# Kernel optimization log

Hardware: AMD Instinct MI355X
Metric: run time of the kernel (lower is better)

Reference implementation:

```python
import jax, jax.numpy as jnp
import numpy as np

B, T, J, D_O = 32, 128, 16, 16
D, H, L, M = 256, 8, 4, 8
DH = D // H
GMAX = 5
MLP = 4 * D
NUM_JOINT = np.array([16, 12, 10, 14, 16, 8, 12, 16])
NUM_GLOBAL = np.array([4, 0, 3, 5, 2, 0, 4, 3])


def setup_inputs() -> dict:
    key = jax.random.key(0)
    it = iter(jax.random.split(key, 48))
    def nrm(shape, s):
        return jax.random.normal(next(it), shape, dtype=jnp.float32) * s
    obs = jax.random.normal(next(it), (B, T, J, D_O), dtype=jnp.float32)
    jtype = jax.random.randint(next(it), (B, T, J), 0, 3)
    slide_mask = jtype == 0
    hinge_mask = jtype == 1
    global_mask = jtype == 2
    act_mask = jax.random.randint(next(it), (B, T, J), 0, 2).astype(bool)
    morph_mask = jax.random.randint(next(it), (B, J, J), 0, 2).astype(bool) | jnp.eye(J, dtype=bool)[None]
    m_idx = jax.random.randint(next(it), (B,), 0, M)
    has_global = jnp.asarray(NUM_GLOBAL > 0)
    s = 0.02
    W_slide = nrm((2, D), s); b_slide = jnp.zeros((D,), jnp.float32)
    W_hinge = nrm((3, D), s); b_hinge = jnp.zeros((D,), jnp.float32)
    # per-morphology global projection, rows beyond num_global zeroed (padding)
    grow = jnp.arange(GMAX)[None, :] < jnp.asarray(NUM_GLOBAL)[:, None]
    W_global = nrm((M, GMAX, D), s) * grow[:, :, None]
    b_global = jnp.zeros((M, D), jnp.float32)
    W_act = nrm((1, D), s)  # actuator_embedding: Linear(1, D, bias=False)
    # per-morphology position embeddings, zero beyond num_joint (matches torch zeros init + slice assign)
    jrow = jnp.arange(J)[None, :] < jnp.asarray(NUM_JOINT)[:, None]
    pos_emb = nrm((M, J, D), 1.0) * jrow[:, :, None]
    ln1_w = jnp.ones((L, D), jnp.float32); ln1_b = jnp.zeros((L, D), jnp.float32)
    qkv_w = nrm((L, D, 3 * D), s); qkv_b = jnp.zeros((L, 3 * D), jnp.float32)
    proj_w = nrm((L, D, D), s); proj_b = jnp.zeros((L, D), jnp.float32)
    ln2_w = jnp.ones((L, D), jnp.float32); ln2_b = jnp.zeros((L, D), jnp.float32)
    fc1_w = nrm((L, D, MLP), s); fc1_b = jnp.zeros((L, MLP), jnp.float32)
    fc2_w = nrm((L, MLP, D), s); fc2_b = jnp.zeros((L, D), jnp.float32)
    ls1 = jnp.full((L, D), 1e-4, jnp.float32); ls2 = jnp.full((L, D), 1e-4, jnp.float32)
    return dict(obs=obs, slide_mask=slide_mask, hinge_mask=hinge_mask, global_mask=global_mask,
                act_mask=act_mask, morph_mask=morph_mask, m_idx=m_idx, has_global=has_global,
                W_slide=W_slide, b_slide=b_slide, W_hinge=W_hinge, b_hinge=b_hinge,
                W_global=W_global, b_global=b_global, W_act=W_act, pos_emb=pos_emb,
                ln1_w=ln1_w, ln1_b=ln1_b, qkv_w=qkv_w, qkv_b=qkv_b, proj_w=proj_w, proj_b=proj_b,
                ln2_w=ln2_w, ln2_b=ln2_b, fc1_w=fc1_w, fc1_b=fc1_b, fc2_w=fc2_w, fc2_b=fc2_b,
                ls1=ls1, ls2=ls2)


def _ln(x, w, b):
    m = x.mean(-1, keepdims=True)
    v = ((x - m) ** 2).mean(-1, keepdims=True)
    return (x - m) * jax.lax.rsqrt(v + 1e-5) * w + b


def reference(obs, slide_mask, hinge_mask, global_mask, act_mask, morph_mask, m_idx, has_global,
              W_slide, b_slide, W_hinge, b_hinge, W_global, b_global, W_act, pos_emb,
              ln1_w, ln1_b, qkv_w, qkv_b, proj_w, proj_b, ln2_w, ln2_b,
              fc1_w, fc1_b, fc2_w, fc2_b, ls1, ls2):
    # --- JointEmbedding (morphology-indexed expert selection, vectorized gather) ---
    emb_slide = obs[..., :2] @ W_slide + b_slide
    x = jnp.where(slide_mask[..., None], emb_slide, jnp.zeros_like(emb_slide))
    emb_hinge = obs[..., :3] @ W_hinge + b_hinge
    x = jnp.where(hinge_mask[..., None], emb_hinge, x)
    # per-sample expert weights gathered by m_idx; padded cols are zero so math matches per-expert in-dims
    emb_g = jnp.einsum('btjg,bgd->btjd', obs[..., :GMAX], W_global[m_idx]) + b_global[m_idx][:, None, None, :]
    gmask = global_mask & has_global[m_idx][:, None, None]  # experts with num_global==0 are skipped
    x = jnp.where(gmask[..., None], emb_g, x)
    # actuator embedding: Linear(1, D, bias=False) on 0/1 mask
    x = x + act_mask[..., None].astype(x.dtype) * W_act[0]
    # morphology-indexed position embedding (zero-padded beyond num_joint)
    x = x + pos_emb[m_idx][:, None]  # (B,1,J,D) broadcast over T
    # --- masked transformer over joints; (B T) flattening == broadcasting mask over T ---
    bias = jnp.where(morph_mask, 0.0, -1e9).astype(x.dtype)[:, None, None, :, :]  # (B,1,1,J,J)
    for l in range(L):
        h = _ln(x, ln1_w[l], ln1_b[l])
        qkv = h @ qkv_w[l] + qkv_b[l]
        q, k, v = jnp.split(qkv, 3, axis=-1)
        def heads(t):
            return t.reshape(B, T, J, H, DH).transpose(0, 1, 3, 2, 4)
        q, k, v = heads(q), heads(k), heads(v)
        scores = jnp.einsum('bthqd,bthkd->bthqk', q, k) * (DH ** -0.5) + bias
        a = jax.nn.softmax(scores, axis=-1)
        o = jnp.einsum('bthqk,bthkd->bthqd', a, v).transpose(0, 1, 3, 2, 4).reshape(B, T, J, D)
        x = x + ls1[l] * (o @ proj_w[l] + proj_b[l])
        h = _ln(x, ln2_w[l], ln2_b[l])
        x = x + ls2[l] * (jax.nn.gelu(h @ fc1_w[l] + fc1_b[l]) @ fc2_w[l] + fc2_b[l])
    return x
```

## Files before the change

### kernel.cpp

```cpp
#include <hip/hip_runtime.h>
#include <hip/hip_bf16.h>
#include <stdint.h>

typedef short bf16x8 __attribute__((ext_vector_type(8)));
typedef float f32x4 __attribute__((ext_vector_type(4)));

#define DI __device__ __forceinline__

DI unsigned short f2bf(float f) {
    return __builtin_bit_cast(unsigned short, __float2bfloat16(f));
}

DI f32x4 mfma16(bf16x8 a, bf16x8 b, f32x4 c) {
    return __builtin_amdgcn_mfma_f32_16x16x32_bf16(a, b, c, 0, 0, 0);
}

DI void gload16(const unsigned short* g, unsigned short* l) {
    __builtin_amdgcn_global_load_lds(
        (const __attribute__((address_space(1))) unsigned int*)g,
        (__attribute__((address_space(3))) unsigned int*)l, 16, 0, 0);
}

DI float gelu_f(float hv) {
    float y = 0.7978845608028654f * (hv + 0.044715f * hv * hv * hv);
    float th = 1.0f - 2.0f / (__expf(2.0f * y) + 1.0f);
    return 0.5f * hv * (1.0f + th);
}

#define RSYNC4() do { asm volatile("s_waitcnt vmcnt(4)" ::: "memory"); \
    __builtin_amdgcn_s_barrier(); __builtin_amdgcn_sched_barrier(0); } while (0)
#define RSYNC0() do { asm volatile("s_waitcnt vmcnt(0)" ::: "memory"); \
    __builtin_amdgcn_s_barrier(); __builtin_amdgcn_sched_barrier(0); } while (0)

__global__ __launch_bounds__(256)
void prep_kernel(const float* __restrict__ qkv_w, const float* __restrict__ proj_w,
                 const float* __restrict__ fc1_w, const float* __restrict__ fc2_w,
                 const float* __restrict__ ls1, const float* __restrict__ ls2,
                 unsigned short* __restrict__ out)
{
    __shared__ float tileA[256][17];
    __shared__ float tileB[32][129];
    const int tid = threadIdx.x;
    const int tgl = blockIdx.x;
    const int layer = tgl / 192;
    const int tl = tgl % 192;
    bool kindA; const float* W; int ldN = 0, src_n16 = 0, strip = 0, ctb = 0;
    const float* lsp = nullptr;
    if (tl < 64) {
        int h = tl >> 3, u = tl & 7;
        if (u < 6) { kindA = true;  W = qkv_w + (size_t)layer * 256 * 768; ldN = 768;
                     src_n16 = (u >> 1) * 16 + 2 * h + (u & 1); }
        else       { kindA = false; W = proj_w + (size_t)layer * 256 * 256; ldN = 256;
                     strip = 32 * h; ctb = (u - 6) * 8; lsp = ls1 + layer * 256; }
    } else {
        int q = tl - 64, rp = q >> 2, v = q & 3;
        if (v < 2) { kindA = true;  W = fc1_w + (size_t)layer * 256 * 1024; ldN = 1024;
                     src_n16 = 2 * rp + v; }
        else       { kindA = false; W = fc2_w + (size_t)layer * 1024 * 256; ldN = 256;
                     strip = 32 * rp; ctb = (v - 2) * 8; lsp = ls2 + layer * 256; }
    }
    if (kindA) {
        const int cn = tid & 15, k0 = tid >> 4;
        const float* src = W + src_n16 * 16 + cn;
        #pragma unroll
        for (int p = 0; p < 16; ++p) {
            int kk = p * 16 + k0;
            tileA[kk][cn] = src[(size_t)kk * ldN];
        }
    } else {
        const int kk = tid >> 3, c0 = (tid & 7) * 16;
        const float* src = W + (size_t)(strip + kk) * ldN + ctb * 16 + c0;
        #pragma unroll
        for (int j = 0; j < 16; ++j) tileB[kk][c0 + j] = src[j];
    }
    __syncthreads();
    unsigned short* dst = out + (size_t)tgl * 4096;
    {
        int e0 = tid * 16;
        int s = e0 >> 9;
        int l = (e0 >> 3) & 63;
        union { unsigned short u[8]; bf16x8 v; } pk;
        if (kindA) {
            int kb = 32 * s + 8 * (l >> 4);
            int n = l & 15;
            #pragma unroll
            for (int i = 0; i < 8; ++i) pk.u[i] = f2bf(tileA[kb + i][n]);
        } else {
            int kb = 8 * (l >> 4);
            int cc = s * 16 + (l & 15);
            const float sc = lsp[ctb * 16 + cc];
            #pragma unroll
            for (int i = 0; i < 8; ++i) pk.u[i] = f2bf(tileB[kb + i][cc] * sc);
        }
        *(bf16x8*)(dst + e0) = pk.v;
        int e1 = e0 + 8;
        int s1 = e1 >> 9;
        int l1 = (e1 >> 3) & 63;
        union { unsigned short u[8]; bf16x8 v; } pk1;
        if (kindA) {
            int kb = 32 * s1 + 8 * (l1 >> 4);
            int n = l1 & 15;
            #pragma unroll
            for (int i = 0; i < 8; ++i) pk1.u[i] = f2bf(tileA[kb + i][n]);
        } else {
            int kb = 8 * (l1 >> 4);
            int cc = s1 * 16 + (l1 & 15);
            const float sc = lsp[ctb * 16 + cc];
            #pragma unroll
            for (int i = 0; i < 8; ++i) pk1.u[i] = f2bf(tileB[kb + i][cc] * sc);
        }
        *(bf16x8*)(dst + e1) = pk1.v;
    }
}

#define CAT_(a, b) a##b
#define CAT(a, b) CAT_(a, b)

#define F8N(F)      F(0)F(1)F(2)F(3)F(4)F(5)F(6)F(7)
#define F16N(F)     F(0)F(1)F(2)F(3)F(4)F(5)F(6)F(7)F(8)F(9)F(10)F(11)F(12)F(13)F(14)F(15)
#define F8A(F,a)    F(0,a)F(1,a)F(2,a)F(3,a)F(4,a)F(5,a)F(6,a)F(7,a)
#define F8H(F,a)    F(8,a)F(9,a)F(10,a)F(11,a)F(12,a)F(13,a)F(14,a)F(15,a)
#define F16A(F,a)   F8A(F,a) F8H(F,a)
#define F8B(F,a,b)  F(0,a,b)F(1,a,b)F(2,a,b)F(3,a,b)F(4,a,b)F(5,a,b)F(6,a,b)F(7,a,b)
#define F16C(F,a,b) F8B(F,a,b) F(8,a,b)F(9,a,b)F(10,a,b)F(11,a,b)F(12,a,b)F(13,a,b)F(14,a,b)F(15,a,b)
#define F16D(F,a,b,c) F(0,a,b,c)F(1,a,b,c)F(2,a,b,c)F(3,a,b,c)F(4,a,b,c)F(5,a,b,c)F(6,a,b,c)F(7,a,b,c)F(8,a,b,c)F(9,a,b,c)F(10,a,b,c)F(11,a,b,c)F(12,a,b,c)F(13,a,b,c)F(14,a,b,c)F(15,a,b,c)

#define DECLX(n)  f32x4 CAT(xA,n);
#define DECLAV(s) bf16x8 CAT(avA,s);

#define EMB_N(n, P, R) { const int col = (n)*16 + lq; float e = 0.f;            \
    if (sl_) e = o0_*W_slide[col] + o1_*W_slide[256+col] + b_slide[col];        \
    else if (hi_) e = o0_*W_hinge[col] + o1_*W_hinge[256+col]                   \
                    + o2_*W_hinge[512+col] + b_hinge[col];                      \
    else if (gl_) e = b_global[m*256+col]                                       \
        + o0_*W_global[(m*5+0)*256+col] + o1_*W_global[(m*5+1)*256+col]         \
        + o2_*W_global[(m*5+2)*256+col] + o3_*W_global[(m*5+3)*256+col]         \
        + o4_*W_global[(m*5+4)*256+col];                                        \
    if (am_) e += W_act[col];                                                   \
    e += pos_emb[pb_ + col];                                                    \
    CAT(CAT(x,P),n)[R] = e; }

#define EMB_ROW(R, G, P) { const int j_ = lg*4 + (R);                           \
    const size_t tok_ = (size_t)(G)*16 + j_;                                    \
    const float* ob_ = obs + tok_*16;                                           \
    const float o0_=ob_[0], o1_=ob_[1], o2_=ob_[2], o3_=ob_[3], o4_=ob_[4];     \
    const int sl_=slide_m[tok_], hi_=hinge_m[tok_];                             \
    const int gl_=global_m[tok_]&&hg; const int am_=act_m[tok_];                \
    const size_t pb_ = ((size_t)m*16+j_)*256;                                   \
    F16C(EMB_N, P, R) }

#define EMBED(G, P) { EMB_ROW(0,G,P) EMB_ROW(1,G,P) EMB_ROW(2,G,P) EMB_ROW(3,G,P) }

#define LNS_N(n, P) { f32x4 v4_ = CAT(CAT(x,P),n);                              \
    sm0+=v4_[0]; sq0+=v4_[0]*v4_[0]; sm1+=v4_[1]; sq1+=v4_[1]*v4_[1];           \
    sm2+=v4_[2]; sq2+=v4_[2]*v4_[2]; sm3+=v4_[3]; sq3+=v4_[3]*v4_[3]; }

#define RED4(v) { v+=__shfl_xor(v,1,64); v+=__shfl_xor(v,2,64);                 \
                  v+=__shfl_xor(v,4,64); v+=__shfl_xor(v,8,64); }

#define LNW_N(n, P) { const float wv_=lw_[(n)*16+lq], lbv_=lb_[(n)*16+lq];      \
    const int t16_=(2*(n)+(lq>>3))&3; const int base_=(((n)&7)>>1)*512+(lq&7);  \
    slotA[base_+(4*lg+0+16*t16_)*8] = f2bf((CAT(CAT(x,P),n)[0]-mu0)*rs0*wv_+lbv_); \
    slotA[base_+(4*lg+1+16*t16_)*8] = f2bf((CAT(CAT(x,P),n)[1]-mu1)*rs1*wv_+lbv_); \
    slotA[base_+(4*lg+2+16*t16_)*8] = f2bf((CAT(CAT(x,P),n)[2]-mu2)*rs2*wv_+lbv_); \
    slotA[base_+(4*lg+3+16*t16_)*8] = f2bf((CAT(CAT(x,P),n)[3]-mu3)*rs3*wv_+lbv_); }

#define LAYER_NORM(LW, LB, P) do {                                              \
    const float* lw_ = (LW); const float* lb_ = (LB);                           \
    float sm0=0,sm1=0,sm2=0,sm3=0, sq0=0,sq1=0,sq2=0,sq3=0;                     \
    F16A(LNS_N, P)                                                              \
    RED4(sm0) RED4(sm1) RED4(sm2) RED4(sm3)                                     \
    RED4(sq0) RED4(sq1) RED4(sq2) RED4(sq3)                                     \
    const float mu0=sm0*(1.f/256.f), mu1=sm1*(1.f/256.f);                       \
    const float mu2=sm2*(1.f/256.f), mu3=sm3*(1.f/256.f);                       \
    const float rs0=rsqrtf(sq0*(1.f/256.f)-mu0*mu0+1e-5f);                      \
    const float rs1=rsqrtf(sq1*(1.f/256.f)-mu1*mu1+1e-5f);                      \
    const float rs2=rsqrtf(sq2*(1.f/256.f)-mu2*mu2+1e-5f);                      \
    const float rs3=rsqrtf(sq3*(1.f/256.f)-mu3*mu3+1e-5f);                      \
    F8A(LNW_N, P)                                                               \
    CAT(CAT(av,P),0) = *(const bf16x8*)(slotA + 0*512 + lane*8);                \
    CAT(CAT(av,P),1) = *(const bf16x8*)(slotA + 1*512 + lane*8);                \
    CAT(CAT(av,P),2) = *(const bf16x8*)(slotA + 2*512 + lane*8);                \
    CAT(CAT(av,P),3) = *(const bf16x8*)(slotA + 3*512 + lane*8);                \
    F8H(LNW_N, P)                                                               \
    CAT(CAT(av,P),4) = *(const bf16x8*)(slotA + 0*512 + lane*8);                \
    CAT(CAT(av,P),5) = *(const bf16x8*)(slotA + 1*512 + lane*8);                \
    CAT(CAT(av,P),6) = *(const bf16x8*)(slotA + 2*512 + lane*8);                \
    CAT(CAT(av,P),7) = *(const bf16x8*)(slotA + 3*512 + lane*8);                \
} while (0)

#define MFKE(s, BUFK, TT) { ae = mfma16(CAT(avA,s), bfrag((BUFK),(TT),(s)), ae); }
#define MFKO(s, BUFK, TT) { aod = mfma16(CAT(avA,s), bfrag((BUFK),(TT),(s)), aod); }
#define MFK8(BUFK, TT) MFKE(0,BUFK,TT) MFKO(1,BUFK,TT) MFKE(2,BUFK,TT) MFKO(3,BUFK,TT) \
                       MFKE(4,BUFK,TT) MFKO(5,BUFK,TT) MFKE(6,BUFK,TT) MFKO(7,BUFK,TT)

#define FOLD_CT(ct, BUFK, OFS, OF) {                                            \
    bf16x8 bq_ = bfrag((BUFK), 2 + ((ct)>>3), (ct)&7);                          \
    CAT(xA,ct) = mfma16((OF), bq_, CAT(xA,ct)); }

#define ADDB_N(n, OFS, BP) { const float d_ = ls_lds[(OFS)+(n)*16+lq]*(BP)[(n)*16+lq]; \
    CAT(xA,n)[0]+=d_; CAT(xA,n)[1]+=d_; CAT(xA,n)[2]+=d_; CAT(xA,n)[3]+=d_; }

#define STORE_N(n) {                                                            \
    op0[(lg*4+0)*256+(n)*16+lq]=CAT(xA,n)[0]; op0[(lg*4+1)*256+(n)*16+lq]=CAT(xA,n)[1]; \
    op0[(lg*4+2)*256+(n)*16+lq]=CAT(xA,n)[2]; op0[(lg*4+3)*256+(n)*16+lq]=CAT(xA,n)[3]; }

__global__ __launch_bounds__(512)
void fused_kernel(const float* __restrict__ obs, const int* __restrict__ slide_m,
                  const int* __restrict__ hinge_m, const int* __restrict__ global_m,
                  const int* __restrict__ act_m, const int* __restrict__ morph_m,
                  const int* __restrict__ m_idx, const int* __restrict__ has_g,
                  const float* __restrict__ W_slide, const float* __restrict__ b_slide,
                  const float* __restrict__ W_hinge, const float* __restrict__ b_hinge,
                  const float* __restrict__ W_global, const float* __restrict__ b_global,
                  const float* __restrict__ W_act, const float* __restrict__ pos_emb,
                  const float* __restrict__ ln1_w, const float* __restrict__ ln1_b,
                  const float* __restrict__ qkv_b, const float* __restrict__ proj_b,
                  const float* __restrict__ ln2_w, const float* __restrict__ ln2_b,
                  const float* __restrict__ fc1_b, const float* __restrict__ fc2_b,
                  const float* __restrict__ ls1, const float* __restrict__ ls2,
                  const unsigned short* __restrict__ wsb, float* __restrict__ out)
{
    __shared__ __align__(16) unsigned char smem[157696];
    unsigned short* dbuf = (unsigned short*)smem;
    float* ls4 = (float*)(smem + 98304);
    float* bias_lds = (float*)(smem + 106496);
    float* biasbuf = (float*)(smem + 107520);
    const int tid = threadIdx.x;
    const int w = tid >> 6, lane = tid & 63, lq = lane & 15, lg = lane >> 4;
    unsigned char* pw = smem + 114688 + w * 5376;
    unsigned short* slotA = (unsigned short*)pw;
    unsigned short* qp = (unsigned short*)pw;
    unsigned short* ks = (unsigned short*)(pw + 1280);
    unsigned short* vT = (unsigned short*)(pw + 2560);

    const int G = blockIdx.x * 8 + w;
    const int b = blockIdx.x >> 4;
    const int m = m_idx[b];
    const int hg = has_g[m];

    if (tid < 256) bias_lds[tid] = morph_m[b * 256 + tid] ? 0.0f : -1e9f;
    #pragma unroll
    for (int l = 0; l < 4; ++l)
        ls4[l * 512 + tid] = (tid < 256) ? ls1[l * 256 + tid] : ls2[l * 256 + tid - 256];

    F16N(DECLX)
    F8N(DECLAV)

    EMBED(G, A)

    auto bfrag = [&](int bufk, int tt, int s) -> bf16x8 {
        return *(const bf16x8*)(dbuf + bufk * 16384 + tt * 4096 + s * 512 + lane * 8);
    };
    auto stage4 = [&](int ri) {
        const unsigned short* src = wsb + (size_t)ri * 16384 + tid * 8;
        unsigned short* dst = dbuf + (ri % 3) * 16384 + tid * 8;
        gload16(src, dst);
        gload16(src + 4096, dst + 4096);
        gload16(src + 8192, dst + 8192);
        gload16(src + 12288, dst + 12288);
    };

    stage4(0);
    stage4(1);
    __syncthreads();

    const float SCALE = 0.17677669529663687f;
    const f32x4 zf = {0.f, 0.f, 0.f, 0.f};

    auto attn = [&]() -> bf16x8 {
        bf16x8 kf = *(const bf16x8*)(ks + lq * 40 + lg * 8);
        bf16x8 qf = *(const bf16x8*)(qp + lq * 40 + lg * 8);
        f32x4 st = mfma16(kf, qf, zf);
        float p0 = st[0] * SCALE + bias_lds[lq * 16 + 4 * lg + 0];
        float p1 = st[1] * SCALE + bias_lds[lq * 16 + 4 * lg + 1];
        float p2 = st[2] * SCALE + bias_lds[lq * 16 + 4 * lg + 2];
        float p3 = st[3] * SCALE + bias_lds[lq * 16 + 4 * lg + 3];
        float mx = fmaxf(fmaxf(p0, p1), fmaxf(p2, p3));
        mx = fmaxf(mx, __shfl_xor(mx, 16, 64));
        mx = fmaxf(mx, __shfl_xor(mx, 32, 64));
        p0 = __expf(p0 - mx); p1 = __expf(p1 - mx);
        p2 = __expf(p2 - mx); p3 = __expf(p3 - mx);
        float ps = p0 + p1 + p2 + p3;
        ps += __shfl_xor(ps, 16, 64);
        ps += __shfl_xor(ps, 32, 64);
        float inv = 1.f / ps;
        qp[lq * 40 + lg * 4 + 0] = f2bf(p0 * inv);
        qp[lq * 40 + lg * 4 + 1] = f2bf(p1 * inv);
        qp[lq * 40 + lg * 4 + 2] = f2bf(p2 * inv);
        qp[lq * 40 + lg * 4 + 3] = f2bf(p3 * inv);
        qp[lq * 40 + 16 + lg * 4 + 0] = 0;
        qp[lq * 40 + 16 + lg * 4 + 1] = 0;
        qp[lq * 40 + 16 + lg * 4 + 2] = 0;
        qp[lq * 40 + 16 + lg * 4 + 3] = 0;
        bf16x8 pf = *(const bf16x8*)(qp + lq * 40 + lg * 8);
        f32x4 o0 = mfma16(pf, *(const bf16x8*)(vT + lq * 40 + lg * 8), zf);
        f32x4 o1 = mfma16(pf, *(const bf16x8*)(vT + (16 + lq) * 40 + lg * 8), zf);
        #pragma unroll
        for (int rr = 0; rr < 4; ++rr) {
            ks[((4 * lg + rr) + 16 * ((lq >> 3) & 3)) * 8 + (lq & 7)] = f2bf(o0[rr]);
            ks[((4 * lg + rr) + 16 * ((2 + (lq >> 3)) & 3)) * 8 + (lq & 7)] = f2bf(o1[rr]);
        }
        return *(const bf16x8*)(ks + lane * 8);
    };

    for (int layer = 0; layer < 4; ++layer) {
        const float* ls_lds = ls4 + layer * 512;

        for (int i = tid; i < 1792; i += 512)
            biasbuf[i] = (i < 768) ? qkv_b[layer * 768 + i]
                                   : fc1_b[layer * 1024 + i - 768];
        __syncthreads();

        LAYER_NORM(ln1_w + layer * 256, ln1_b + layer * 256, A);
        #pragma unroll
        for (int ii = 0; ii < 8; ++ii) {
            int idx = ii * 64 + lane;
            vT[(idx >> 4) * 40 + 16 + (idx & 15)] = 0;
        }
        { const float* pbp_ = proj_b + layer * 256; F16C(ADDB_N, 0, pbp_) }

        for (int r = 0; r < 16; ++r) {
            const int rg = layer * 48 + r;
            RSYNC4();
            if (rg + 2 <= 191) stage4(rg + 2);
            const int bufk = rg % 3;
            const int h = r >> 1;
            if (!(r & 1)) {
                #pragma unroll
                for (int tt = 0; tt < 4; ++tt) {
                    int sec = tt >> 1, nn = tt & 1;
                    float bv = biasbuf[sec * 256 + (2 * h + nn) * 16 + lq];
                    f32x4 ae = {bv, bv, bv, bv}, aod = zf;
                    MFK8(bufk, tt)
                    f32x4 a0 = ae + aod;
                    unsigned short* dstl = sec ? ks : qp;
                    #pragma unroll
                    for (int rr = 0; rr < 4; ++rr)
                        dstl[(4 * lg + rr) * 40 + nn * 16 + lq] = f2bf(a0[rr]);
                }
            } else {
                #pragma unroll
                for (int tt = 0; tt < 2; ++tt) {
                    float bv = biasbuf[512 + (2 * h + tt) * 16 + lq];
                    f32x4 ae = {bv, bv, bv, bv}, aod = zf;
                    MFK8(bufk, tt)
                    f32x4 a0 = ae + aod;
                    #pragma unroll
                    for (int rr = 0; rr < 4; ++rr)
                        vT[(tt * 16 + lq) * 40 + 4 * lg + rr] = f2bf(a0[rr]);
                }
                bf16x8 of = attn();
                F16D(FOLD_CT, bufk, 0, of)
            }
        }

        LAYER_NORM(ln2_w + layer * 256, ln2_b + layer * 256, A);
        { const float* pbf_ = fc2_b + layer * 256; F16C(ADDB_N, 256, pbf_) }

        for (int r2 = 0; r2 < 32; ++r2) {
            const int rg = layer * 48 + 16 + r2;
            if (rg == 191) { RSYNC0(); } else { RSYNC4(); }
            if (rg + 2 <= 191) stage4(rg + 2);
            const int bufk = rg % 3;
            #pragma unroll
            for (int tt = 0; tt < 2; ++tt) {
                float bv = biasbuf[768 + (2 * r2 + tt) * 16 + lq];
                f32x4 ae = {bv, bv, bv, bv}, aod = zf;
                MFK8(bufk, tt)
                f32x4 a0 = ae + aod;
                int t16 = (2 * tt + (lq >> 3)) & 3;
                #pragma unroll
                for (int rr = 0; rr < 4; ++rr)
                    ks[((4 * lg + rr) + 16 * t16) * 8 + (lq & 7)] = f2bf(gelu_f(a0[rr]));
            }
            bf16x8 gf = *(const bf16x8*)(ks + lane * 8);
            F16D(FOLD_CT, bufk, 256, gf)
        }
    }

    float* op0 = out + (size_t)G * 4096;
    F16N(STORE_N)
}

extern "C" void kernel_launch(void* const* d_in, const int* in_sizes, int n_in,
                              void* d_out, int out_size, void* d_ws, size_t ws_size,
                              hipStream_t stream) {
    (void)in_sizes; (void)n_in; (void)out_size; (void)ws_size;
    const float* obs      = (const float*)d_in[0];
    const int*   slide_m  = (const int*)d_in[1];
    const int*   hinge_m  = (const int*)d_in[2];
    const int*   global_m = (const int*)d_in[3];
    const int*   act_m    = (const int*)d_in[4];
    const int*   morph_m  = (const int*)d_in[5];
    const int*   m_idx    = (const int*)d_in[6];
    const int*   has_g    = (const int*)d_in[7];
    const float* W_slide  = (const float*)d_in[8];
    const float* b_slide  = (const float*)d_in[9];
    const float* W_hinge  = (const float*)d_in[10];
    const float* b_hinge  = (const float*)d_in[11];
    const float* W_global = (const float*)d_in[12];
    const float* b_global = (const float*)d_in[13];
    const float* W_act    = (const float*)d_in[14];
    const float* pos_emb  = (const float*)d_in[15];
    const float* ln1_w    = (const float*)d_in[16];
    const float* ln1_b    = (const float*)d_in[17];
    const float* qkv_w    = (const float*)d_in[18];
    const float* qkv_b    = (const float*)d_in[19];
    const float* proj_w   = (const float*)d_in[20];
    const float* proj_b   = (const float*)d_in[21];
    const float* ln2_w    = (const float*)d_in[22];
    const float* ln2_b    = (const float*)d_in[23];
    const float* fc1_w    = (const float*)d_in[24];
    const float* fc1_b    = (const float*)d_in[25];
    const float* fc2_w    = (const float*)d_in[26];
    const float* fc2_b    = (const float*)d_in[27];
    const float* ls1      = (const float*)d_in[28];
    const float* ls2      = (const float*)d_in[29];
    unsigned short* wsb = (unsigned short*)d_ws;

    prep_kernel<<<768, 256, 0, stream>>>(qkv_w, proj_w, fc1_w, fc2_w, ls1, ls2, wsb);
    fused_kernel<<<512, 512, 0, stream>>>(obs, slide_m, hinge_m, global_m, act_m, morph_m,
        m_idx, has_g, W_slide, b_slide, W_hinge, b_hinge, W_global, b_global, W_act, pos_emb,
        ln1_w, ln1_b, qkv_b, proj_b, ln2_w, ln2_b, fc1_b, fc2_b, ls1, ls2, wsb, (float*)d_out);
}
```

Before: 769.4 us.

## Process two token groups per wave to reuse staged weight fragments

```diff
diff --git a/kernel.cpp b/kernel.cpp
--- a/kernel.cpp
+++ b/kernel.cpp
@@ -27,9 +27,7 @@
     return 0.5f * hv * (1.0f + th);
 }
 
-#define RSYNC4() do { asm volatile("s_waitcnt vmcnt(4)" ::: "memory"); \
-    __builtin_amdgcn_s_barrier(); __builtin_amdgcn_sched_barrier(0); } while (0)
-#define RSYNC0() do { asm volatile("s_waitcnt vmcnt(0)" ::: "memory"); \
+#define RSYNC() do { asm volatile("s_waitcnt vmcnt(0)" ::: "memory"); \
     __builtin_amdgcn_s_barrier(); __builtin_amdgcn_sched_barrier(0); } while (0)
 
 __global__ __launch_bounds__(256)
@@ -125,8 +123,8 @@
 #define F16C(F,a,b) F8B(F,a,b) F(8,a,b)F(9,a,b)F(10,a,b)F(11,a,b)F(12,a,b)F(13,a,b)F(14,a,b)F(15,a,b)
 #define F16D(F,a,b,c) F(0,a,b,c)F(1,a,b,c)F(2,a,b,c)F(3,a,b,c)F(4,a,b,c)F(5,a,b,c)F(6,a,b,c)F(7,a,b,c)F(8,a,b,c)F(9,a,b,c)F(10,a,b,c)F(11,a,b,c)F(12,a,b,c)F(13,a,b,c)F(14,a,b,c)F(15,a,b,c)
 
-#define DECLX(n)  f32x4 CAT(xA,n);
-#define DECLAV(s) bf16x8 CAT(avA,s);
+#define DECLX(n)  f32x4 CAT(xA,n), CAT(xB,n);
+#define DECLAV(s) bf16x8 CAT(avA,s), CAT(avB,s);
 
 #define EMB_N(n, P, R) { const int col = (n)*16 + lq; float e = 0.f;            \
     if (sl_) e = o0_*W_slide[col] + o1_*W_slide[256+col] + b_slide[col];        \
@@ -189,23 +187,28 @@
     CAT(CAT(av,P),7) = *(const bf16x8*)(slotA + 3*512 + lane*8);                \
 } while (0)
 
-#define MFKE(s, BUFK, TT) { ae = mfma16(CAT(avA,s), bfrag((BUFK),(TT),(s)), ae); }
-#define MFKO(s, BUFK, TT) { aod = mfma16(CAT(avA,s), bfrag((BUFK),(TT),(s)), aod); }
-#define MFK8(BUFK, TT) MFKE(0,BUFK,TT) MFKO(1,BUFK,TT) MFKE(2,BUFK,TT) MFKO(3,BUFK,TT) \
-                       MFKE(4,BUFK,TT) MFKO(5,BUFK,TT) MFKE(6,BUFK,TT) MFKO(7,BUFK,TT)
-
-#define FOLD_CT(ct, BUFK, OFS, OF) {                                            \
+#define MFKD(s, BUFK, TT) { bf16x8 bq_ = bfrag((BUFK),(TT),(s));                \
+    a0 = mfma16(CAT(avA,s), bq_, a0); a1 = mfma16(CAT(avB,s), bq_, a1); }
+#define MFK8D(BUFK, TT) MFKD(0,BUFK,TT) MFKD(1,BUFK,TT) MFKD(2,BUFK,TT) MFKD(3,BUFK,TT) \
+                        MFKD(4,BUFK,TT) MFKD(5,BUFK,TT) MFKD(6,BUFK,TT) MFKD(7,BUFK,TT)
+
+#define FOLDD_CT(ct, BUFK, OFA, OFB) {                                          \
     bf16x8 bq_ = bfrag((BUFK), 2 + ((ct)>>3), (ct)&7);                          \
-    CAT(xA,ct) = mfma16((OF), bq_, CAT(xA,ct)); }
-
-#define ADDB_N(n, OFS, BP) { const float d_ = ls_lds[(OFS)+(n)*16+lq]*(BP)[(n)*16+lq]; \
-    CAT(xA,n)[0]+=d_; CAT(xA,n)[1]+=d_; CAT(xA,n)[2]+=d_; CAT(xA,n)[3]+=d_; }
-
-#define STORE_N(n) {                                                            \
+    CAT(xA,ct) = mfma16((OFA), bq_, CAT(xA,ct));                                \
+    CAT(xB,ct) = mfma16((OFB), bq_, CAT(xB,ct)); }
+
+#define ADDBD_N(n, OFS) { const float d_ = biasbuf[(OFS)+(n)*16+lq];            \
+    CAT(xA,n)[0]+=d_; CAT(xA,n)[1]+=d_; CAT(xA,n)[2]+=d_; CAT(xA,n)[3]+=d_;     \
+    CAT(xB,n)[0]+=d_; CAT(xB,n)[1]+=d_; CAT(xB,n)[2]+=d_; CAT(xB,n)[3]+=d_; }
+
+#define STORED_N(n) {                                                           \
     op0[(lg*4+0)*256+(n)*16+lq]=CAT(xA,n)[0]; op0[(lg*4+1)*256+(n)*16+lq]=CAT(xA,n)[1]; \
-    op0[(lg*4+2)*256+(n)*16+lq]=CAT(xA,n)[2]; op0[(lg*4+3)*256+(n)*16+lq]=CAT(xA,n)[3]; }
-
-__global__ __launch_bounds__(512)
+    op0[(lg*4+2)*256+(n)*16+lq]=CAT(xA,n)[2]; op0[(lg*4+3)*256+(n)*16+lq]=CAT(xA,n)[3]; \
+    op1[(lg*4+0)*256+(n)*16+lq]=CAT(xB,n)[0]; op1[(lg*4+1)*256+(n)*16+lq]=CAT(xB,n)[1]; \
+    op1[(lg*4+2)*256+(n)*16+lq]=CAT(xB,n)[2]; op1[(lg*4+3)*256+(n)*16+lq]=CAT(xB,n)[3]; }
+
+__global__
+__attribute__((amdgpu_flat_work_group_size(512, 512), amdgpu_waves_per_eu(1, 2)))
 void fused_kernel(const float* __restrict__ obs, const int* __restrict__ slide_m,
                   const int* __restrict__ hinge_m, const int* __restrict__ global_m,
                   const int* __restrict__ act_m, const int* __restrict__ morph_m,
@@ -223,38 +226,30 @@
 {
     __shared__ __align__(16) unsigned char smem[157696];
     unsigned short* dbuf = (unsigned short*)smem;
-    float* ls4 = (float*)(smem + 98304);
-    float* bias_lds = (float*)(smem + 106496);
-    float* biasbuf = (float*)(smem + 107520);
+    float* bias_lds = (float*)(smem + 65536);
+    float* biasbuf = (float*)(smem + 66560);
     const int tid = threadIdx.x;
     const int w = tid >> 6, lane = tid & 63, lq = lane & 15, lg = lane >> 4;
-    unsigned char* pw = smem + 114688 + w * 5376;
+    unsigned char* pw = smem + 75776 + w * 10240;
     unsigned short* slotA = (unsigned short*)pw;
-    unsigned short* qp = (unsigned short*)pw;
-    unsigned short* ks = (unsigned short*)(pw + 1280);
-    unsigned short* vT = (unsigned short*)(pw + 2560);
-
-    const int G = blockIdx.x * 8 + w;
-    const int b = blockIdx.x >> 4;
+    unsigned short* qp0 = (unsigned short*)pw;
+    unsigned short* ks0 = (unsigned short*)(pw + 1280);
+    unsigned short* vT0 = (unsigned short*)(pw + 2560);
+    unsigned short* qp1 = (unsigned short*)(pw + 5120);
+    unsigned short* ks1 = (unsigned short*)(pw + 6400);
+    unsigned short* vT1 = (unsigned short*)(pw + 7680);
+
+    const int G0 = blockIdx.x * 16 + 2 * w;
+    const int b = blockIdx.x >> 3;
     const int m = m_idx[b];
     const int hg = has_g[m];
-
-    if (tid < 256) bias_lds[tid] = morph_m[b * 256 + tid] ? 0.0f : -1e9f;
-    #pragma unroll
-    for (int l = 0; l < 4; ++l)
-        ls4[l * 512 + tid] = (tid < 256) ? ls1[l * 256 + tid] : ls2[l * 256 + tid - 256];
-
-    F16N(DECLX)
-    F8N(DECLAV)
-
-    EMBED(G, A)
 
     auto bfrag = [&](int bufk, int tt, int s) -> bf16x8 {
         return *(const bf16x8*)(dbuf + bufk * 16384 + tt * 4096 + s * 512 + lane * 8);
     };
     auto stage4 = [&](int ri) {
         const unsigned short* src = wsb + (size_t)ri * 16384 + tid * 8;
-        unsigned short* dst = dbuf + (ri % 3) * 16384 + tid * 8;
+        unsigned short* dst = dbuf + (ri & 1) * 16384 + tid * 8;
         gload16(src, dst);
         gload16(src + 4096, dst + 4096);
         gload16(src + 8192, dst + 8192);
@@ -262,13 +257,25 @@
     };
 
     stage4(0);
-    stage4(1);
-    __syncthreads();
+    if (tid < 256) bias_lds[tid] = morph_m[b * 256 + tid] ? 0.0f : -1e9f;
+    #pragma unroll
+    for (int ii = 0; ii < 8; ++ii) {
+        int idx = ii * 64 + lane;
+        int row = idx >> 4, c = idx & 15;
+        vT0[row * 40 + 16 + c] = 0;
+        vT1[row * 40 + 16 + c] = 0;
+    }
+
+    F16N(DECLX)
+    F8N(DECLAV)
+
+    EMBED(G0, A)
+    EMBED(G0 + 1, B)
 
     const float SCALE = 0.17677669529663687f;
     const f32x4 zf = {0.f, 0.f, 0.f, 0.f};
 
-    auto attn = [&]() -> bf16x8 {
+    auto attn = [&](unsigned short* qp, unsigned short* ks, unsigned short* vT) -> bf16x8 {
         bf16x8 kf = *(const bf16x8*)(ks + lq * 40 + lg * 8);
         bf16x8 qf = *(const bf16x8*)(qp + lq * 40 + lg * 8);
         f32x4 st = mfma16(kf, qf, zf);
@@ -305,82 +312,94 @@
     };
 
     for (int layer = 0; layer < 4; ++layer) {
-        const float* ls_lds = ls4 + layer * 512;
-
-        for (int i = tid; i < 1792; i += 512)
-            biasbuf[i] = (i < 768) ? qkv_b[layer * 768 + i]
-                                   : fc1_b[layer * 1024 + i - 768];
+        for (int i = tid; i < 2304; i += 512) {
+            float v;
+            if (i < 768)       v = qkv_b[layer * 768 + i];
+            else if (i < 1792) v = fc1_b[layer * 1024 + i - 768];
+            else if (i < 2048) v = ls1[layer * 256 + i - 1792] * proj_b[layer * 256 + i - 1792];
+            else               v = ls2[layer * 256 + i - 2048] * fc2_b[layer * 256 + i - 2048];
+            biasbuf[i] = v;
+        }
         __syncthreads();
 
         LAYER_NORM(ln1_w + layer * 256, ln1_b + layer * 256, A);
+        LAYER_NORM(ln1_w + layer * 256, ln1_b + layer * 256, B);
         #pragma unroll
         for (int ii = 0; ii < 8; ++ii) {
             int idx = ii * 64 + lane;
-            vT[(idx >> 4) * 40 + 16 + (idx & 15)] = 0;
-        }
-        { const float* pbp_ = proj_b + layer * 256; F16C(ADDB_N, 0, pbp_) }
+            vT0[(idx >> 4) * 40 + 16 + (idx & 15)] = 0;
+        }
+        F16A(ADDBD_N, 1792)
 
         for (int r = 0; r < 16; ++r) {
             const int rg = layer * 48 + r;
-            RSYNC4();
-            if (rg + 2 <= 191) stage4(rg + 2);
-            const int bufk = rg % 3;
+            RSYNC();
+            if (rg + 1 < 192) stage4(rg + 1);
+            const int bufk = rg & 1;
             const int h = r >> 1;
             if (!(r & 1)) {
                 #pragma unroll
                 for (int tt = 0; tt < 4; ++tt) {
                     int sec = tt >> 1, nn = tt & 1;
                     float bv = biasbuf[sec * 256 + (2 * h + nn) * 16 + lq];
-                    f32x4 ae = {bv, bv, bv, bv}, aod = zf;
-                    MFK8(bufk, tt)
-                    f32x4 a0 = ae + aod;
-                    unsigned short* dstl = sec ? ks : qp;
+                    f32x4 a0 = {bv, bv, bv, bv}, a1 = a0;
+                    MFK8D(bufk, tt)
+                    unsigned short* d0 = sec ? ks0 : qp0;
+                    unsigned short* d1 = sec ? ks1 : qp1;
                     #pragma unroll
-                    for (int rr = 0; rr < 4; ++rr)
-                        dstl[(4 * lg + rr) * 40 + nn * 16 + lq] = f2bf(a0[rr]);
+                    for (int rr = 0; rr < 4; ++rr) {
+                        d0[(4 * lg + rr) * 40 + nn * 16 + lq] = f2bf(a0[rr]);
+                        d1[(4 * lg + rr) * 40 + nn * 16 + lq] = f2bf(a1[rr]);
+                    }
                 }
             } else {
                 #pragma unroll
                 for (int tt = 0; tt < 2; ++tt) {
                     float bv = biasbuf[512 + (2 * h + tt) * 16 + lq];
-                    f32x4 ae = {bv, bv, bv, bv}, aod = zf;
-                    MFK8(bufk, tt)
-                    f32x4 a0 = ae + aod;
+                    f32x4 a0 = {bv, bv, bv, bv}, a1 = a0;
+                    MFK8D(bufk, tt)
                     #pragma unroll
-                    for (int rr = 0; rr < 4; ++rr)
-                        vT[(tt * 16 + lq) * 40 + 4 * lg + rr] = f2bf(a0[rr]);
+                    for (int rr = 0; rr < 4; ++rr) {
+                        vT0[(tt * 16 + lq) * 40 + 4 * lg + rr] = f2bf(a0[rr]);
+                        vT1[(tt * 16 + lq) * 40 + 4 * lg + rr] = f2bf(a1[rr]);
+                    }
                 }
-                bf16x8 of = attn();
-                F16D(FOLD_CT, bufk, 0, of)
+                bf16x8 ofA = attn(qp0, ks0, vT0);
+                bf16x8 ofB = attn(qp1, ks1, vT1);
+                F16D(FOLDD_CT, bufk, ofA, ofB)
             }
         }
 
         LAYER_NORM(ln2_w + layer * 256, ln2_b + layer * 256, A);
-        { const float* pbf_ = fc2_b + layer * 256; F16C(ADDB_N, 256, pbf_) }
+        LAYER_NORM(ln2_w + layer * 256, ln2_b + layer * 256, B);
+        F16A(ADDBD_N, 2048)
 
         for (int r2 = 0; r2 < 32; ++r2) {
             const int rg = layer * 48 + 16 + r2;
-            if (rg == 191) { RSYNC0(); } else { RSYNC4(); }
-            if (rg + 2 <= 191) stage4(rg + 2);
-            const int bufk = rg % 3;
+            RSYNC();
+            if (rg + 1 < 192) stage4(rg + 1);
+            const int bufk = rg & 1;
             #pragma unroll
             for (int tt = 0; tt < 2; ++tt) {
                 float bv = biasbuf[768 + (2 * r2 + tt) * 16 + lq];
-                f32x4 ae = {bv, bv, bv, bv}, aod = zf;
-                MFK8(bufk, tt)
-                f32x4 a0 = ae + aod;
+                f32x4 a0 = {bv, bv, bv, bv}, a1 = a0;
+                MFK8D(bufk, tt)
                 int t16 = (2 * tt + (lq >> 3)) & 3;
                 #pragma unroll
-                for (int rr = 0; rr < 4; ++rr)
-                    ks[((4 * lg + rr) + 16 * t16) * 8 + (lq & 7)] = f2bf(gelu_f(a0[rr]));
+                for (int rr = 0; rr < 4; ++rr) {
+                    ks0[((4 * lg + rr) + 16 * t16) * 8 + (lq & 7)] = f2bf(gelu_f(a0[rr]));
+                    ks1[((4 * lg + rr) + 16 * t16) * 8 + (lq & 7)] = f2bf(gelu_f(a1[rr]));
+                }
             }
-            bf16x8 gf = *(const bf16x8*)(ks + lane * 8);
-            F16D(FOLD_CT, bufk, 256, gf)
+            bf16x8 gfA = *(const bf16x8*)(ks0 + lane * 8);
+            bf16x8 gfB = *(const bf16x8*)(ks1 + lane * 8);
+            F16D(FOLDD_CT, bufk, gfA, gfB)
         }
     }
 
-    float* op0 = out + (size_t)G * 4096;
-    F16N(STORE_N)
+    float* op0 = out + (size_t)G0 * 4096;
+    float* op1 = op0 + 4096;
+    F16N(STORED_N)
 }
 
 extern "C" void kernel_launch(void* const* d_in, const int* in_sizes, int n_in,
@@ -420,7 +439,7 @@
     unsigned short* wsb = (unsigned short*)d_ws;
 
     prep_kernel<<<768, 256, 0, stream>>>(qkv_w, proj_w, fc1_w, fc2_w, ls1, ls2, wsb);
-    fused_kernel<<<512, 512, 0, stream>>>(obs, slide_m, hinge_m, global_m, act_m, morph_m,
+    fused_kernel<<<256, 512, 0, stream>>>(obs, slide_m, hinge_m, global_m, act_m, morph_m,
         m_idx, has_g, W_slide, b_slide, W_hinge, b_hinge, W_global, b_global, W_act, pos_emb,
         ln1_w, ln1_b, qkv_b, proj_b, ln2_w, ln2_b, fc1_b, fc2_b, ls1, ls2, wsb, (float*)d_out);
 }
```

Result: slower. 1.232 ms (+60.1%).

## Use FP8 MFMA for QKV and FC1 projections with repacked weight staging

Applied to the files above, without the earlier changes.

```diff
diff --git a/kernel.cpp b/kernel.cpp
--- a/kernel.cpp
+++ b/kernel.cpp
@@ -11,11 +11,20 @@
     return __builtin_bit_cast(unsigned short, __float2bfloat16(f));
 }
 
+DI unsigned char f2fp8(float f) {
+    int p = __builtin_amdgcn_cvt_pk_fp8_f32(f, 0.f, 0, false);
+    return (unsigned char)(p & 0xff);
+}
+
 DI f32x4 mfma16(bf16x8 a, bf16x8 b, f32x4 c) {
     return __builtin_amdgcn_mfma_f32_16x16x32_bf16(a, b, c, 0, 0, 0);
 }
 
-DI void gload16(const unsigned short* g, unsigned short* l) {
+DI f32x4 mfma8(long a, long b, f32x4 c) {
+    return __builtin_amdgcn_mfma_f32_16x16x32_fp8_fp8(a, b, c, 0, 0, 0);
+}
+
+DI void gload16c(const unsigned char* g, unsigned char* l) {
     __builtin_amdgcn_global_load_lds(
         (const __attribute__((address_space(1))) unsigned int*)g,
         (__attribute__((address_space(3))) unsigned int*)l, 16, 0, 0);
@@ -27,16 +36,14 @@
     return 0.5f * hv * (1.0f + th);
 }
 
-#define RSYNC4() do { asm volatile("s_waitcnt vmcnt(4)" ::: "memory"); \
-    __builtin_amdgcn_s_barrier(); __builtin_amdgcn_sched_barrier(0); } while (0)
-#define RSYNC0() do { asm volatile("s_waitcnt vmcnt(0)" ::: "memory"); \
+#define RSYNCN(N) do { asm volatile("s_waitcnt vmcnt(" #N ")" ::: "memory"); \
     __builtin_amdgcn_s_barrier(); __builtin_amdgcn_sched_barrier(0); } while (0)
 
 __global__ __launch_bounds__(256)
 void prep_kernel(const float* __restrict__ qkv_w, const float* __restrict__ proj_w,
                  const float* __restrict__ fc1_w, const float* __restrict__ fc2_w,
                  const float* __restrict__ ls1, const float* __restrict__ ls2,
-                 unsigned short* __restrict__ out)
+                 unsigned char* __restrict__ out)
 {
     __shared__ float tileA[256][17];
     __shared__ float tileB[32][129];
@@ -46,19 +53,25 @@
     const int tl = tgl % 192;
     bool kindA; const float* W; int ldN = 0, src_n16 = 0, strip = 0, ctb = 0;
     const float* lsp = nullptr;
+    size_t off;
     if (tl < 64) {
         int h = tl >> 3, u = tl & 7;
         if (u < 6) { kindA = true;  W = qkv_w + (size_t)layer * 256 * 768; ldN = 768;
-                     src_n16 = (u >> 1) * 16 + 2 * h + (u & 1); }
+                     src_n16 = (u >> 1) * 16 + 2 * h + (u & 1);
+                     off = (size_t)h * 40960 + (u < 4 ? u * 4096 : 16384 + (u - 4) * 4096); }
         else       { kindA = false; W = proj_w + (size_t)layer * 256 * 256; ldN = 256;
-                     strip = 32 * h; ctb = (u - 6) * 8; lsp = ls1 + layer * 256; }
+                     strip = 32 * h; ctb = (u - 6) * 8; lsp = ls1 + layer * 256;
+                     off = (size_t)h * 40960 + 24576 + (size_t)(u - 6) * 8192; }
     } else {
         int q = tl - 64, rp = q >> 2, v = q & 3;
         if (v < 2) { kindA = true;  W = fc1_w + (size_t)layer * 256 * 1024; ldN = 1024;
-                     src_n16 = 2 * rp + v; }
+                     src_n16 = 2 * rp + v;
+                     off = 327680 + (size_t)rp * 24576 + (size_t)v * 4096; }
         else       { kindA = false; W = fc2_w + (size_t)layer * 1024 * 256; ldN = 256;
-                     strip = 32 * rp; ctb = (v - 2) * 8; lsp = ls2 + layer * 256; }
+                     strip = 32 * rp; ctb = (v - 2) * 8; lsp = ls2 + layer * 256;
+                     off = 327680 + (size_t)rp * 24576 + 8192 + (size_t)(v - 2) * 8192; }
     }
+    off += (size_t)layer * 1114112;
     if (kindA) {
         const int cn = tid & 15, k0 = tid >> 4;
         const float* src = W + src_n16 * 16 + cn;
@@ -74,42 +87,46 @@
         for (int j = 0; j < 16; ++j) tileB[kk][c0 + j] = src[j];
     }
     __syncthreads();
-    unsigned short* dst = out + (size_t)tgl * 4096;
-    {
+    if (kindA) {
+        unsigned char* dstb = out + off;
+        int e0 = tid * 16;
+        int s = e0 >> 9;
+        int l = (e0 >> 3) & 63;
+        union { unsigned char u[8]; unsigned long long v; } g0, g1;
+        int kb0 = 32 * s + 8 * (l >> 4), n0 = l & 15;
+        int kb1 = 32 * s + 8 * ((l + 1) >> 4), n1 = (l + 1) & 15;
+        #pragma unroll
+        for (int i = 0; i < 8; ++i) g0.u[i] = f2fp8(tileA[kb0 + i][n0]);
+        #pragma unroll
+        for (int i = 0; i < 8; ++i) g1.u[i] = f2fp8(tileA[kb1 + i][n1]);
+        *(unsigned long long*)(dstb + e0) = g0.v;
+        *(unsigned long long*)(dstb + e0 + 8) = g1.v;
+    } else {
+        unsigned short* dsts = (unsigned short*)(out + off);
         int e0 = tid * 16;
         int s = e0 >> 9;
         int l = (e0 >> 3) & 63;
         union { unsigned short u[8]; bf16x8 v; } pk;
-        if (kindA) {
-            int kb = 32 * s + 8 * (l >> 4);
-            int n = l & 15;
-            #pragma unroll
-            for (int i = 0; i < 8; ++i) pk.u[i] = f2bf(tileA[kb + i][n]);
-        } else {
+        {
             int kb = 8 * (l >> 4);
             int cc = s * 16 + (l & 15);
             const float sc = lsp[ctb * 16 + cc];
             #pragma unroll
             for (int i = 0; i < 8; ++i) pk.u[i] = f2bf(tileB[kb + i][cc] * sc);
-        }
-        *(bf16x8*)(dst + e0) = pk.v;
+            *(bf16x8*)(dsts + e0) = pk.v;
+        }
         int e1 = e0 + 8;
         int s1 = e1 >> 9;
         int l1 = (e1 >> 3) & 63;
         union { unsigned short u[8]; bf16x8 v; } pk1;
-        if (kindA) {
-            int kb = 32 * s1 + 8 * (l1 >> 4);
-            int n = l1 & 15;
-            #pragma unroll
-            for (int i = 0; i < 8; ++i) pk1.u[i] = f2bf(tileA[kb + i][n]);
-        } else {
+        {
             int kb = 8 * (l1 >> 4);
             int cc = s1 * 16 + (l1 & 15);
             const float sc = lsp[ctb * 16 + cc];
             #pragma unroll
             for (int i = 0; i < 8; ++i) pk1.u[i] = f2bf(tileB[kb + i][cc] * sc);
-        }
-        *(bf16x8*)(dst + e1) = pk1.v;
+            *(bf16x8*)(dsts + e1) = pk1.v;
+        }
     }
 }
 
@@ -123,10 +140,9 @@
 #define F16A(F,a)   F8A(F,a) F8H(F,a)
 #define F8B(F,a,b)  F(0,a,b)F(1,a,b)F(2,a,b)F(3,a,b)F(4,a,b)F(5,a,b)F(6,a,b)F(7,a,b)
 #define F16C(F,a,b) F8B(F,a,b) F(8,a,b)F(9,a,b)F(10,a,b)F(11,a,b)F(12,a,b)F(13,a,b)F(14,a,b)F(15,a,b)
-#define F16D(F,a,b,c) F(0,a,b,c)F(1,a,b,c)F(2,a,b,c)F(3,a,b,c)F(4,a,b,c)F(5,a,b,c)F(6,a,b,c)F(7,a,b,c)F(8,a,b,c)F(9,a,b,c)F(10,a,b,c)F(11,a,b,c)F(12,a,b,c)F(13,a,b,c)F(14,a,b,c)F(15,a,b,c)
 
 #define DECLX(n)  f32x4 CAT(xA,n);
-#define DECLAV(s) bf16x8 CAT(avA,s);
+#define DECLAV(s) long CAT(avA,s);
 
 #define EMB_N(n, P, R) { const int col = (n)*16 + lq; float e = 0.f;            \
     if (sl_) e = o0_*W_slide[col] + o1_*W_slide[256+col] + b_slide[col];        \
@@ -160,10 +176,10 @@
 
 #define LNW_N(n, P) { const float wv_=lw_[(n)*16+lq], lbv_=lb_[(n)*16+lq];      \
     const int t16_=(2*(n)+(lq>>3))&3; const int base_=(((n)&7)>>1)*512+(lq&7);  \
-    slotA[base_+(4*lg+0+16*t16_)*8] = f2bf((CAT(CAT(x,P),n)[0]-mu0)*rs0*wv_+lbv_); \
-    slotA[base_+(4*lg+1+16*t16_)*8] = f2bf((CAT(CAT(x,P),n)[1]-mu1)*rs1*wv_+lbv_); \
-    slotA[base_+(4*lg+2+16*t16_)*8] = f2bf((CAT(CAT(x,P),n)[2]-mu2)*rs2*wv_+lbv_); \
-    slotA[base_+(4*lg+3+16*t16_)*8] = f2bf((CAT(CAT(x,P),n)[3]-mu3)*rs3*wv_+lbv_); }
+    slotA8[base_+(4*lg+0+16*t16_)*8] = f2fp8((CAT(CAT(x,P),n)[0]-mu0)*rs0*wv_+lbv_); \
+    slotA8[base_+(4*lg+1+16*t16_)*8] = f2fp8((CAT(CAT(x,P),n)[1]-mu1)*rs1*wv_+lbv_); \
+    slotA8[base_+(4*lg+2+16*t16_)*8] = f2fp8((CAT(CAT(x,P),n)[2]-mu2)*rs2*wv_+lbv_); \
+    slotA8[base_+(4*lg+3+16*t16_)*8] = f2fp8((CAT(CAT(x,P),n)[3]-mu3)*rs3*wv_+lbv_); }
 
 #define LAYER_NORM(LW, LB, P) do {                                              \
     const float* lw_ = (LW); const float* lb_ = (LB);                           \
@@ -178,27 +194,27 @@
     const float rs2=rsqrtf(sq2*(1.f/256.f)-mu2*mu2+1e-5f);                      \
     const float rs3=rsqrtf(sq3*(1.f/256.f)-mu3*mu3+1e-5f);                      \
     F8A(LNW_N, P)                                                               \
-    CAT(CAT(av,P),0) = *(const bf16x8*)(slotA + 0*512 + lane*8);                \
-    CAT(CAT(av,P),1) = *(const bf16x8*)(slotA + 1*512 + lane*8);                \
-    CAT(CAT(av,P),2) = *(const bf16x8*)(slotA + 2*512 + lane*8);                \
-    CAT(CAT(av,P),3) = *(const bf16x8*)(slotA + 3*512 + lane*8);                \
+    CAT(CAT(av,P),0) = *(const long*)(slotA8 + 0*512 + lane*8);                 \
+    CAT(CAT(av,P),1) = *(const long*)(slotA8 + 1*512 + lane*8);                 \
+    CAT(CAT(av,P),2) = *(const long*)(slotA8 + 2*512 + lane*8);                 \
+    CAT(CAT(av,P),3) = *(const long*)(slotA8 + 3*512 + lane*8);                 \
     F8H(LNW_N, P)                                                               \
-    CAT(CAT(av,P),4) = *(const bf16x8*)(slotA + 0*512 + lane*8);                \
-    CAT(CAT(av,P),5) = *(const bf16x8*)(slotA + 1*512 + lane*8);                \
-    CAT(CAT(av,P),6) = *(const bf16x8*)(slotA + 2*512 + lane*8);                \
-    CAT(CAT(av,P),7) = *(const bf16x8*)(slotA + 3*512 + lane*8);                \
+    CAT(CAT(av,P),4) = *(const long*)(slotA8 + 0*512 + lane*8);                 \
+    CAT(CAT(av,P),5) = *(const long*)(slotA8 + 1*512 + lane*8);                 \
+    CAT(CAT(av,P),6) = *(const long*)(slotA8 + 2*512 + lane*8);                 \
+    CAT(CAT(av,P),7) = *(const long*)(slotA8 + 3*512 + lane*8);                 \
 } while (0)
 
-#define MFKE(s, BUFK, TT) { ae = mfma16(CAT(avA,s), bfrag((BUFK),(TT),(s)), ae); }
-#define MFKO(s, BUFK, TT) { aod = mfma16(CAT(avA,s), bfrag((BUFK),(TT),(s)), aod); }
-#define MFK8(BUFK, TT) MFKE(0,BUFK,TT) MFKO(1,BUFK,TT) MFKE(2,BUFK,TT) MFKO(3,BUFK,TT) \
-                       MFKE(4,BUFK,TT) MFKO(5,BUFK,TT) MFKE(6,BUFK,TT) MFKO(7,BUFK,TT)
-
-#define FOLD_CT(ct, BUFK, OFS, OF) {                                            \
-    bf16x8 bq_ = bfrag((BUFK), 2 + ((ct)>>3), (ct)&7);                          \
+#define MFKE(s, BUFK, TT) { ae = mfma8(CAT(avA,s), bfragW8((BUFK),(TT),(s)), ae); }
+#define MFKO(s, BUFK, TT) { aod = mfma8(CAT(avA,s), bfragW8((BUFK),(TT),(s)), aod); }
+#define MFK8F(BUFK, TT) MFKE(0,BUFK,TT) MFKO(1,BUFK,TT) MFKE(2,BUFK,TT) MFKO(3,BUFK,TT) \
+                        MFKE(4,BUFK,TT) MFKO(5,BUFK,TT) MFKE(6,BUFK,TT) MFKO(7,BUFK,TT)
+
+#define FOLD_CT(ct, BUFK, OF) {                                                 \
+    bf16x8 bq_ = bfragStrip((BUFK), (ct));                                      \
     CAT(xA,ct) = mfma16((OF), bq_, CAT(xA,ct)); }
 
-#define ADDB_N(n, OFS, BP) { const float d_ = ls_lds[(OFS)+(n)*16+lq]*(BP)[(n)*16+lq]; \
+#define ADDB_N(n, OFS) { const float d_ = biasbuf[(OFS)+(n)*16+lq];             \
     CAT(xA,n)[0]+=d_; CAT(xA,n)[1]+=d_; CAT(xA,n)[2]+=d_; CAT(xA,n)[3]+=d_; }
 
 #define STORE_N(n) {                                                            \
@@ -219,17 +235,16 @@
                   const float* __restrict__ ln2_w, const float* __restrict__ ln2_b,
                   const float* __restrict__ fc1_b, const float* __restrict__ fc2_b,
                   const float* __restrict__ ls1, const float* __restrict__ ls2,
-                  const unsigned short* __restrict__ wsb, float* __restrict__ out)
+                  const unsigned char* __restrict__ wsb, float* __restrict__ out)
 {
-    __shared__ __align__(16) unsigned char smem[157696];
-    unsigned short* dbuf = (unsigned short*)smem;
-    float* ls4 = (float*)(smem + 98304);
-    float* bias_lds = (float*)(smem + 106496);
-    float* biasbuf = (float*)(smem + 107520);
+    __shared__ __align__(16) unsigned char smem[126976];
+    unsigned char* dbuf = smem;
+    float* bias_lds = (float*)(smem + 73728);
+    float* biasbuf = (float*)(smem + 74752);
     const int tid = threadIdx.x;
     const int w = tid >> 6, lane = tid & 63, lq = lane & 15, lg = lane >> 4;
-    unsigned char* pw = smem + 114688 + w * 5376;
-    unsigned short* slotA = (unsigned short*)pw;
+    unsigned char* pw = smem + 83968 + w * 5376;
+    unsigned char* slotA8 = pw;
     unsigned short* qp = (unsigned short*)pw;
     unsigned short* ks = (unsigned short*)(pw + 1280);
     unsigned short* vT = (unsigned short*)(pw + 2560);
@@ -239,31 +254,41 @@
     const int m = m_idx[b];
     const int hg = has_g[m];
 
+    auto bfragW8 = [&](int bufk, int tile, int s) -> long {
+        return *(const long*)(dbuf + bufk * 24576 + tile * 4096 + s * 512 + lane * 8);
+    };
+    auto bfragStrip = [&](int bufk, int ct) -> bf16x8 {
+        return *(const bf16x8*)(dbuf + bufk * 24576 + 8192 + (ct >> 3) * 8192
+                                + (ct & 7) * 1024 + lane * 16);
+    };
+    auto stageRound = [&](int ri) {
+        int lyr = ri / 48, rr = ri - lyr * 48;
+        size_t off; int nld;
+        if (rr < 16) { off = (size_t)lyr * 1114112 + (size_t)(rr >> 1) * 40960
+                           + (size_t)(rr & 1) * 16384;
+                       nld = (rr & 1) ? 3 : 2; }
+        else         { off = (size_t)lyr * 1114112 + 327680 + (size_t)(rr - 16) * 24576;
+                       nld = 3; }
+        const unsigned char* src = wsb + off + tid * 16;
+        unsigned char* dst = dbuf + (ri % 3) * 24576 + tid * 16;
+        gload16c(src, dst);
+        gload16c(src + 8192, dst + 8192);
+        if (nld == 3) gload16c(src + 16384, dst + 16384);
+    };
+
+    stageRound(0);
+    stageRound(1);
     if (tid < 256) bias_lds[tid] = morph_m[b * 256 + tid] ? 0.0f : -1e9f;
     #pragma unroll
-    for (int l = 0; l < 4; ++l)
-        ls4[l * 512 + tid] = (tid < 256) ? ls1[l * 256 + tid] : ls2[l * 256 + tid - 256];
+    for (int ii = 0; ii < 8; ++ii) {
+        int idx = ii * 64 + lane;
+        vT[(idx >> 4) * 40 + 16 + (idx & 15)] = 0;
+    }
 
     F16N(DECLX)
     F8N(DECLAV)
 
     EMBED(G, A)
-
-    auto bfrag = [&](int bufk, int tt, int s) -> bf16x8 {
-        return *(const bf16x8*)(dbuf + bufk * 16384 + tt * 4096 + s * 512 + lane * 8);
-    };
-    auto stage4 = [&](int ri) {
-        const unsigned short* src = wsb + (size_t)ri * 16384 + tid * 8;
-        unsigned short* dst = dbuf + (ri % 3) * 16384 + tid * 8;
-        gload16(src, dst);
-        gload16(src + 4096, dst + 4096);
-        gload16(src + 8192, dst + 8192);
-        gload16(src + 12288, dst + 12288);
-    };
-
-    stage4(0);
-    stage4(1);
-    __syncthreads();
 
     const float SCALE = 0.17677669529663687f;
     const f32x4 zf = {0.f, 0.f, 0.f, 0.f};
@@ -305,11 +330,14 @@
     };
 
     for (int layer = 0; layer < 4; ++layer) {
-        const float* ls_lds = ls4 + layer * 512;
-
-        for (int i = tid; i < 1792; i += 512)
-            biasbuf[i] = (i < 768) ? qkv_b[layer * 768 + i]
-                                   : fc1_b[layer * 1024 + i - 768];
+        for (int i = tid; i < 2304; i += 512) {
+            float v;
+            if (i < 768)       v = qkv_b[layer * 768 + i];
+            else if (i < 1792) v = fc1_b[layer * 1024 + i - 768];
+            else if (i < 2048) v = ls1[layer * 256 + i - 1792] * proj_b[layer * 256 + i - 1792];
+            else               v = ls2[layer * 256 + i - 2048] * fc2_b[layer * 256 + i - 2048];
+            biasbuf[i] = v;
+        }
         __syncthreads();
 
         LAYER_NORM(ln1_w + layer * 256, ln1_b + layer * 256, A);
@@ -318,21 +346,21 @@
             int idx = ii * 64 + lane;
             vT[(idx >> 4) * 40 + 16 + (idx & 15)] = 0;
         }
-        { const float* pbp_ = proj_b + layer * 256; F16C(ADDB_N, 0, pbp_) }
+        F16A(ADDB_N, 1792)
 
         for (int r = 0; r < 16; ++r) {
             const int rg = layer * 48 + r;
-            RSYNC4();
-            if (rg + 2 <= 191) stage4(rg + 2);
             const int bufk = rg % 3;
             const int h = r >> 1;
             if (!(r & 1)) {
+                RSYNCN(3);
+                if (rg + 2 <= 191) stageRound(rg + 2);
                 #pragma unroll
                 for (int tt = 0; tt < 4; ++tt) {
                     int sec = tt >> 1, nn = tt & 1;
                     float bv = biasbuf[sec * 256 + (2 * h + nn) * 16 + lq];
                     f32x4 ae = {bv, bv, bv, bv}, aod = zf;
-                    MFK8(bufk, tt)
+                    MFK8F(bufk, tt)
                     f32x4 a0 = ae + aod;
                     unsigned short* dstl = sec ? ks : qp;
                     #pragma unroll
@@ -340,34 +368,38 @@
                         dstl[(4 * lg + rr) * 40 + nn * 16 + lq] = f2bf(a0[rr]);
                 }
             } else {
+                if (r != 15) { RSYNCN(2); } else { RSYNCN(3); }
+                if (rg + 2 <= 191) stageRound(rg + 2);
                 #pragma unroll
                 for (int tt = 0; tt < 2; ++tt) {
                     float bv = biasbuf[512 + (2 * h + tt) * 16 + lq];
                     f32x4 ae = {bv, bv, bv, bv}, aod = zf;
-                    MFK8(bufk, tt)
+                    MFK8F(bufk, tt)
                     f32x4 a0 = ae + aod;
                     #pragma unroll
                     for (int rr = 0; rr < 4; ++rr)
                         vT[(tt * 16 + lq) * 40 + 4 * lg + rr] = f2bf(a0[rr]);
                 }
                 bf16x8 of = attn();
-                F16D(FOLD_CT, bufk, 0, of)
+                F16C(FOLD_CT, bufk, of)
             }
         }
 
         LAYER_NORM(ln2_w + layer * 256, ln2_b + layer * 256, A);
-        { const float* pbf_ = fc2_b + layer * 256; F16C(ADDB_N, 256, pbf_) }
+        F16A(ADDB_N, 2048)
 
         for (int r2 = 0; r2 < 32; ++r2) {
             const int rg = layer * 48 + 16 + r2;
-            if (rg == 191) { RSYNC0(); } else { RSYNC4(); }
-            if (rg + 2 <= 191) stage4(rg + 2);
             const int bufk = rg % 3;
+            if (r2 != 31)       { RSYNCN(3); }
+            else if (rg != 191) { RSYNCN(2); }
+            else                { RSYNCN(0); }
+            if (rg + 2 <= 191) stageRound(rg + 2);
             #pragma unroll
             for (int tt = 0; tt < 2; ++tt) {
                 float bv = biasbuf[768 + (2 * r2 + tt) * 16 + lq];
                 f32x4 ae = {bv, bv, bv, bv}, aod = zf;
-                MFK8(bufk, tt)
+                MFK8F(bufk, tt)
                 f32x4 a0 = ae + aod;
                 int t16 = (2 * tt + (lq >> 3)) & 3;
                 #pragma unroll
@@ -375,7 +407,7 @@
                     ks[((4 * lg + rr) + 16 * t16) * 8 + (lq & 7)] = f2bf(gelu_f(a0[rr]));
             }
             bf16x8 gf = *(const bf16x8*)(ks + lane * 8);
-            F16D(FOLD_CT, bufk, 256, gf)
+            F16C(FOLD_CT, bufk, gf)
         }
     }
 
@@ -417,7 +449,7 @@
     const float* fc2_b    = (const float*)d_in[27];
     const float* ls1      = (const float*)d_in[28];
     const float* ls2      = (const float*)d_in[29];
-    unsigned short* wsb = (unsigned short*)d_ws;
+    unsigned char* wsb = (unsigned char*)d_ws;
 
     prep_kernel<<<768, 256, 0, stream>>>(qkv_w, proj_w, fc1_w, fc2_w, ls1, ls2, wsb);
     fused_kernel<<<512, 512, 0, stream>>>(obs, slide_m, hinge_m, global_m, act_m, morph_m,
```

Measured after the change: 717.5 us. 1.07x faster.
